# Optimization experiments

Hardware: AMD Instinct MI355X
Metric: run time of the kernel (lower is better)

## Reference

```python
import jax, jax.numpy as jnp
import numpy as np

N_QUBITS = 8
DEPTH = 3
FEATURE_DIM = 512
NUM_CLASSES = 10
BATCH = 8192
CDTYPE = jnp.complex64


def _ry_batched(theta):
    # theta: (B,) -> (B,2,2) real RY matrices cast to complex
    c = jnp.cos(theta / 2)
    s = jnp.sin(theta / 2)
    row0 = jnp.stack([c, -s], axis=-1)
    row1 = jnp.stack([s, c], axis=-1)
    return jnp.stack([row0, row1], axis=-2).astype(CDTYPE)


def _ry(theta):
    c = jnp.cos(theta / 2).astype(CDTYPE)
    s = jnp.sin(theta / 2).astype(CDTYPE)
    return jnp.stack([jnp.stack([c, -s]), jnp.stack([s, c])])


def _rx(theta):
    c = jnp.cos(theta / 2).astype(CDTYPE)
    js = (-1j) * jnp.sin(theta / 2).astype(CDTYPE)
    return jnp.stack([jnp.stack([c, js]), jnp.stack([js, c])])


def _apply_1q(state, U, q, n):
    # state: (B, 2,...,2) little-endian: axis (n - q) holds qubit q's bit
    ax = n - q
    sm = jnp.moveaxis(state, ax, -1)
    if U.ndim == 3:  # per-batch gate
        new = jnp.einsum('b...k,bjk->b...j', sm, U)
    else:  # shared gate
        new = jnp.einsum('...k,jk->...j', sm, U)
    return jnp.moveaxis(new, -1, ax)


def _cnot(state, c, t, n):
    ax_c = n - c
    ax_t = n - t
    s0, s1 = jnp.split(state, 2, axis=ax_c)
    s1 = jnp.flip(s1, axis=ax_t)  # X on target where control=1
    return jnp.concatenate([s0, s1], axis=ax_c)


def _quantum_expect(angles, qnn_w, n=N_QUBITS, depth=DEPTH):
    # angles: (B, n) encoding angles; qnn_w: (depth*n*3,) circuit weights
    B = angles.shape[0]
    state = jnp.zeros((B,) + (2,) * n, CDTYPE)
    state = state.at[(slice(None),) + (0,) * n].set(1.0)
    # RY encoding layer (batched angles)
    for q in range(n):
        state = _apply_1q(state, _ry_batched(angles[:, q]), q, n)
    wr = qnn_w.reshape(depth, n, 3)
    for l in range(depth):
        for q in range(n):
            state = _apply_1q(state, _rx(wr[l, q, 0]), q, n)
            state = _apply_1q(state, _ry(wr[l, q, 1]), q, n)
            state = _apply_1q(state, _rx(wr[l, q, 2]), q, n)
        for q in range(n - 1):
            state = _cnot(state, q, q + 1, n)
        state = _cnot(state, n - 1, 0, n)
    # PauliZ expectation per qubit: sum probs weighted by (+1, -1) on that qubit's axis
    p = state.real ** 2 + state.imag ** 2  # (B, 2,...,2) real
    z = jnp.array([1.0, -1.0], p.dtype)
    outs = []
    for q in range(n):
        ax = n - q
        sign = z.reshape((1,) * ax + (2,) + (1,) * q)
        outs.append(jnp.sum(p * sign, axis=tuple(range(1, n + 1))))
    return jnp.stack(outs, axis=-1)  # (B, n)


def setup_inputs() -> dict:
    key = jax.random.key(0)
    k1, k2, k3, k4, k5 = jax.random.split(key, 5)
    x = jax.random.normal(k1, (BATCH, FEATURE_DIM), jnp.float32)
    bound_p = 1.0 / np.sqrt(FEATURE_DIM)
    proj_w = jax.random.uniform(k2, (N_QUBITS, FEATURE_DIM), jnp.float32, -bound_p, bound_p)
    qnn_w = 0.01 * jax.random.normal(k3, (DEPTH * N_QUBITS * 3,), jnp.float32)
    bound_o = 1.0 / np.sqrt(N_QUBITS)
    out_w = jax.random.uniform(k4, (NUM_CLASSES, N_QUBITS), jnp.float32, -bound_o, bound_o)
    out_b = jax.random.uniform(k5, (NUM_CLASSES,), jnp.float32, -bound_o, bound_o)
    return {'x': x, 'proj_w': proj_w, 'qnn_w': qnn_w, 'out_w': out_w, 'out_b': out_b}


def reference(x, proj_w, qnn_w, out_w, out_b):
    angles = jnp.tanh(x @ proj_w.T) * (jnp.pi / 2)  # (B, n_qubits)
    q_out = _quantum_expect(angles, qnn_w)          # (B, n_qubits)
    return q_out @ out_w.T + out_b                  # (B, num_classes)
```

## Files before the change

### kernel.cpp

```cpp
#include <hip/hip_runtime.h>
#include <math.h>

#define NQ 8
#define NDEPTH 3
#define FEAT 512
#define NCLS 10
#define NBATCH 8192

__global__ void gate_precompute(const float* __restrict__ qnn_w,
                                float* __restrict__ gates) {
    int i = threadIdx.x;
    if (i < NDEPTH * NQ) {
        float t0 = 0.5f * qnn_w[i * 3 + 0];
        float t1 = 0.5f * qnn_w[i * 3 + 1];
        float t2 = 0.5f * qnn_w[i * 3 + 2];
        float c0 = cosf(t0), s0 = sinf(t0);
        float c1 = cosf(t1), s1 = sinf(t1);
        float c2 = cosf(t2), s2 = sinf(t2);
        float m00r =  c1 * c0, m00i =  s1 * s0;
        float m01r = -s1 * c0, m01i = -c1 * s0;
        float m10r =  s1 * c0, m10i = -c1 * s0;
        float m11r =  c1 * c0, m11i = -s1 * s0;
        float* g = gates + i * 8;
        g[0] =  c2 * m00r + s2 * m10i;  g[1] =  c2 * m00i - s2 * m10r;
        g[2] =  c2 * m01r + s2 * m11i;  g[3] =  c2 * m01i - s2 * m11r;
        g[4] =  s2 * m00i + c2 * m10r;  g[5] = -s2 * m00r + c2 * m10i;
        g[6] =  s2 * m01i + c2 * m11r;  g[7] = -s2 * m01r + c2 * m11i;
    }
}

template <int CTRL, int ROW_MASK>
__device__ __forceinline__ float dpp_term(float v) {
    return __int_as_float(__builtin_amdgcn_update_dpp(
        0, __float_as_int(v), CTRL, ROW_MASK, 0xf, true));
}

__device__ __forceinline__ float wave_sum_bcast(float v) {
    v += dpp_term<0x111, 0xf>(v);
    v += dpp_term<0x112, 0xf>(v);
    v += dpp_term<0x114, 0xf>(v);
    v += dpp_term<0x118, 0xf>(v);
    v += dpp_term<0x142, 0xa>(v);
    v += dpp_term<0x143, 0xc>(v);
    return __int_as_float(__builtin_amdgcn_readlane(__float_as_int(v), 63));
}

__device__ __forceinline__ float bcastlane(float v, int srclane) {
    return __int_as_float(__builtin_amdgcn_readlane(__float_as_int(v), srclane));
}

template <int CTRL>
__device__ __forceinline__ float dpp_xor(float v) {
    return __int_as_float(__builtin_amdgcn_update_dpp(
        0, __float_as_int(v), CTRL, 0xf, 0xf, true));
}

__device__ __forceinline__ float fast_tanh(float v) {
    float e = __expf(2.f * v);
    return 1.f - 2.f / (e + 1.f);
}


__device__ __forceinline__ void cgate_pair(const float* __restrict__ u,
        float& r0, float& i0, float& r1, float& i1) {
    float nr0 = u[0]*r0 - u[1]*i0 + u[2]*r1 - u[3]*i1;
    float ni0 = u[0]*i0 + u[1]*r0 + u[2]*i1 + u[3]*r1;
    float nr1 = u[4]*r0 - u[5]*i0 + u[6]*r1 - u[7]*i1;
    float ni1 = u[4]*i0 + u[5]*r0 + u[6]*i1 + u[7]*r1;
    r0 = nr0; i0 = ni0; r1 = nr1; i1 = ni1;
}

__device__ __forceinline__ void cgate_shfl(const float* __restrict__ u, int bit,
        int mask, float (&re)[4], float (&im)[4]) {
    float dr  = bit ? u[6] : u[0], di = bit ? u[7] : u[1];
    float orr = bit ? u[4] : u[2], oi = bit ? u[5] : u[3];
#pragma unroll
    for (int j = 0; j < 4; j++) {
        float pr = __shfl_xor(re[j], mask);
        float pi = __shfl_xor(im[j], mask);
        float nr = dr*re[j] - di*im[j] + orr*pr - oi*pi;
        float ni = dr*im[j] + di*re[j] + orr*pi + oi*pr;
        re[j] = nr; im[j] = ni;
    }
}

template <int CTRL>
__device__ __forceinline__ void cgate_dpp(const float* __restrict__ u, int bit,
        float (&re)[4], float (&im)[4]) {
    float dr  = bit ? u[6] : u[0], di = bit ? u[7] : u[1];
    float orr = bit ? u[4] : u[2], oi = bit ? u[5] : u[3];
#pragma unroll
    for (int j = 0; j < 4; j++) {
        float pr = dpp_xor<CTRL>(re[j]);
        float pi = dpp_xor<CTRL>(im[j]);
        float nr = dr*re[j] - di*im[j] + orr*pr - oi*pi;
        float ni = dr*im[j] + di*re[j] + orr*pi + oi*pr;
        re[j] = nr; im[j] = ni;
    }
}

__global__ __launch_bounds__(256) void qsim_kernel(
        const float* __restrict__ x, const float* __restrict__ proj_w,
        const float* __restrict__ gates, const float* __restrict__ out_w,
        const float* __restrict__ out_b, float* __restrict__ out) {
    int tid  = threadIdx.x;
    int lane = tid & 63;
    int b    = blockIdx.x * 4 + (tid >> 6);

    const float4* xr4 = (const float4*)(x + (size_t)b * FEAT);
    float4 xa = xr4[lane], xb = xr4[lane + 64];
    float dq[8];
#pragma unroll
    for (int q = 0; q < 8; q++) {
        const float4* pw4 = (const float4*)(proj_w + q * FEAT);
        float4 wa = pw4[lane], wb = pw4[lane + 64];
        float acc = xa.x*wa.x + xa.y*wa.y + xa.z*wa.z + xa.w*wa.w
                  + xb.x*wb.x + xb.y*wb.y + xb.z*wb.z + xb.w*wb.w;
        dq[q] = wave_sum_bcast(acc);
    }
    int qsel = lane >> 3;
    float a0 = (qsel & 4) ? dq[4] : dq[0];
    float a1 = (qsel & 4) ? dq[5] : dq[1];
    float a2 = (qsel & 4) ? dq[6] : dq[2];
    float a3 = (qsel & 4) ? dq[7] : dq[3];
    float b0 = (qsel & 2) ? a2 : a0;
    float b1 = (qsel & 2) ? a3 : a1;
    float dsel = (qsel & 1) ? b1 : b0;
    float th = fast_tanh(dsel) * 0.78539816339744830962f;
    float se = __sinf(th), ce = __cosf(th);
    float cq[8], sq[8];
#pragma unroll
    for (int q = 0; q < 8; q++) {
        cq[q] = bcastlane(ce, q * 8);
        sq[q] = bcastlane(se, q * 8);
    }

    float F = 1.f;
#pragma unroll
    for (int q = 2; q < 8; q++) {
        int bit = (lane >> (q - 2)) & 1;
        F *= bit ? sq[q] : cq[q];
    }
    float re[4], im[4];
    re[0] = F * cq[0] * cq[1];
    re[1] = F * sq[0] * cq[1];
    re[2] = F * cq[0] * sq[1];
    re[3] = F * sq[0] * sq[1];
    im[0] = im[1] = im[2] = im[3] = 0.f;

#pragma unroll
    for (int l = 0; l < NDEPTH; l++) {
        const float* g = gates + l * NQ * 8;
        cgate_pair(g, re[0], im[0], re[1], im[1]);
        cgate_pair(g, re[2], im[2], re[3], im[3]);
        cgate_pair(g + 8,  re[0], im[0], re[2], im[2]);
        cgate_pair(g + 8,  re[1], im[1], re[3], im[3]);
        cgate_dpp<0xB1>(g + 16, lane & 1,        re, im);
        cgate_dpp<0x4E>(g + 24, (lane >> 1) & 1, re, im);
        cgate_shfl(g + 32, (lane >> 2) & 1, 4,  re, im);
        cgate_shfl(g + 40, (lane >> 3) & 1, 8,  re, im);
        cgate_shfl(g + 48, (lane >> 4) & 1, 16, re, im);
        cgate_shfl(g + 56, (lane >> 5) & 1, 32, re, im);

        { float t = re[1]; re[1] = re[3]; re[3] = t;
          t = im[1]; im[1] = im[3]; im[3] = t; }
        int base  = lane ^ ((lane << 1) & 63);
        int base2 = base ^ 1;
        re[0] = __shfl(re[0], base);  im[0] = __shfl(im[0], base);
        re[1] = __shfl(re[1], base);  im[1] = __shfl(im[1], base);
        re[2] = __shfl(re[2], base2); im[2] = __shfl(im[2], base2);
        re[3] = __shfl(re[3], base2); im[3] = __shfl(im[3], base2);
        int bit5 = (lane >> 5) & 1;
        {
            float t0 = bit5 ? re[1] : re[0], t1 = bit5 ? re[0] : re[1];
            float t2 = bit5 ? re[3] : re[2], t3 = bit5 ? re[2] : re[3];
            re[0] = t0; re[1] = t1; re[2] = t2; re[3] = t3;
            t0 = bit5 ? im[1] : im[0]; t1 = bit5 ? im[0] : im[1];
            t2 = bit5 ? im[3] : im[2]; t3 = bit5 ? im[2] : im[3];
            im[0] = t0; im[1] = t1; im[2] = t2; im[3] = t3;
        }
    }

    float p0 = re[0]*re[0] + im[0]*im[0];
    float p1 = re[1]*re[1] + im[1]*im[1];
    float p2 = re[2]*re[2] + im[2]*im[2];
    float p3 = re[3]*re[3] + im[3]*im[3];
    float pt = p0 + p1 + p2 + p3;
    float eq[8];
    eq[0] = wave_sum_bcast(p0 - p1 + p2 - p3);
    eq[1] = wave_sum_bcast(p0 + p1 - p2 - p3);
#pragma unroll
    for (int q = 2; q < 8; q++) {
        int bit = (lane >> (q - 2)) & 1;
        eq[q] = wave_sum_bcast(bit ? -pt : pt);
    }

    if (lane < NCLS) {
        const float* wrow = out_w + lane * NQ;
        float acc = out_b[lane];
#pragma unroll
        for (int q = 0; q < 8; q++) acc = fmaf(eq[q], wrow[q], acc);
        out[(size_t)b * NCLS + lane] = acc;
    }
}

extern "C" void kernel_launch(void* const* d_in, const int* in_sizes, int n_in,
                              void* d_out, int out_size, void* d_ws, size_t ws_size,
                              hipStream_t stream) {
    const float* x      = (const float*)d_in[0];
    const float* proj_w = (const float*)d_in[1];
    const float* qnn_w  = (const float*)d_in[2];
    const float* out_w  = (const float*)d_in[3];
    const float* out_b  = (const float*)d_in[4];
    float* out   = (float*)d_out;
    float* gates = (float*)d_ws;

    gate_precompute<<<1, 64, 0, stream>>>(qnn_w, gates);
    qsim_kernel<<<NBATCH / 4, 256, 0, stream>>>(x, proj_w, gates, out_w, out_b, out);
}
```

Baseline: 85.56 us.

## Recast circuit as 256x256 unitary matrix applied via fp16 MFMA GEMM

Splits the fused simulation into four kernels. The first writes product-state encodings to a workspace in fp16. The second builds the full 256x256 circuit unitary by simulating each basis state. The third multiplies the encodings by the unitary's real and imaginary parts on MFMA, then folds the probabilities straight into class logits through a precomputed sign table. This moves the per-sample gate shuffles onto matrix cores, but adds extra launches, a workspace round trip, and fp16 rounding of both the state and the unitary.

```diff
diff --git a/kernel.cpp b/kernel.cpp
--- a/kernel.cpp
+++ b/kernel.cpp
@@ -7,8 +7,14 @@
 #define NCLS 10
 #define NBATCH 8192
 
-__global__ void gate_precompute(const float* __restrict__ qnn_w,
-                                float* __restrict__ gates) {
+typedef _Float16 v8h __attribute__((ext_vector_type(8)));
+typedef _Float16 v4h __attribute__((ext_vector_type(4)));
+typedef float v4f __attribute__((ext_vector_type(4)));
+
+
+__global__ void precompute(const float* __restrict__ qnn_w,
+                           const float* __restrict__ out_w,
+                           float* __restrict__ gates, float* __restrict__ T) {
     int i = threadIdx.x;
     if (i < NDEPTH * NQ) {
         float t0 = 0.5f * qnn_w[i * 3 + 0];
@@ -27,6 +33,16 @@
         g[4] =  s2 * m00i + c2 * m10r;  g[5] = -s2 * m00r + c2 * m10i;
         g[6] =  s2 * m01i + c2 * m11r;  g[7] = -s2 * m01r + c2 * m11i;
     }
+    if (i < 256) {
+#pragma unroll
+        for (int c = 0; c < NCLS; c++) {
+            float s = 0.f;
+#pragma unroll
+            for (int q = 0; q < NQ; q++)
+                s += (((i >> q) & 1) ? -1.f : 1.f) * out_w[c * NQ + q];
+            T[i * NCLS + c] = s;
+        }
+    }
 }
 
 template <int CTRL, int ROW_MASK>
@@ -60,7 +76,6 @@
     return 1.f - 2.f / (e + 1.f);
 }
 
-
 __device__ __forceinline__ void cgate_pair(const float* __restrict__ u,
         float& r0, float& i0, float& r1, float& i1) {
     float nr0 = u[0]*r0 - u[1]*i0 + u[2]*r1 - u[3]*i1;
@@ -99,55 +114,8 @@
     }
 }
 
-__global__ __launch_bounds__(256) void qsim_kernel(
-        const float* __restrict__ x, const float* __restrict__ proj_w,
-        const float* __restrict__ gates, const float* __restrict__ out_w,
-        const float* __restrict__ out_b, float* __restrict__ out) {
-    int tid  = threadIdx.x;
-    int lane = tid & 63;
-    int b    = blockIdx.x * 4 + (tid >> 6);
-
-    const float4* xr4 = (const float4*)(x + (size_t)b * FEAT);
-    float4 xa = xr4[lane], xb = xr4[lane + 64];
-    float dq[8];
-#pragma unroll
-    for (int q = 0; q < 8; q++) {
-        const float4* pw4 = (const float4*)(proj_w + q * FEAT);
-        float4 wa = pw4[lane], wb = pw4[lane + 64];
-        float acc = xa.x*wa.x + xa.y*wa.y + xa.z*wa.z + xa.w*wa.w
-                  + xb.x*wb.x + xb.y*wb.y + xb.z*wb.z + xb.w*wb.w;
-        dq[q] = wave_sum_bcast(acc);
-    }
-    int qsel = lane >> 3;
-    float a0 = (qsel & 4) ? dq[4] : dq[0];
-    float a1 = (qsel & 4) ? dq[5] : dq[1];
-    float a2 = (qsel & 4) ? dq[6] : dq[2];
-    float a3 = (qsel & 4) ? dq[7] : dq[3];
-    float b0 = (qsel & 2) ? a2 : a0;
-    float b1 = (qsel & 2) ? a3 : a1;
-    float dsel = (qsel & 1) ? b1 : b0;
-    float th = fast_tanh(dsel) * 0.78539816339744830962f;
-    float se = __sinf(th), ce = __cosf(th);
-    float cq[8], sq[8];
-#pragma unroll
-    for (int q = 0; q < 8; q++) {
-        cq[q] = bcastlane(ce, q * 8);
-        sq[q] = bcastlane(se, q * 8);
-    }
-
-    float F = 1.f;
-#pragma unroll
-    for (int q = 2; q < 8; q++) {
-        int bit = (lane >> (q - 2)) & 1;
-        F *= bit ? sq[q] : cq[q];
-    }
-    float re[4], im[4];
-    re[0] = F * cq[0] * cq[1];
-    re[1] = F * sq[0] * cq[1];
-    re[2] = F * cq[0] * sq[1];
-    re[3] = F * sq[0] * sq[1];
-    im[0] = im[1] = im[2] = im[3] = 0.f;
-
+__device__ __forceinline__ void apply_circuit(const float* __restrict__ gates,
+        int lane, float (&re)[4], float (&im)[4]) {
 #pragma unroll
     for (int l = 0; l < NDEPTH; l++) {
         const float* g = gates + l * NQ * 8;
@@ -161,7 +129,6 @@
         cgate_shfl(g + 40, (lane >> 3) & 1, 8,  re, im);
         cgate_shfl(g + 48, (lane >> 4) & 1, 16, re, im);
         cgate_shfl(g + 56, (lane >> 5) & 1, 32, re, im);
-
         { float t = re[1]; re[1] = re[3]; re[3] = t;
           t = im[1]; im[1] = im[3]; im[3] = t; }
         int base  = lane ^ ((lane << 1) & 63);
@@ -180,27 +147,143 @@
             im[0] = t0; im[1] = t1; im[2] = t2; im[3] = t3;
         }
     }
-
-    float p0 = re[0]*re[0] + im[0]*im[0];
-    float p1 = re[1]*re[1] + im[1]*im[1];
-    float p2 = re[2]*re[2] + im[2]*im[2];
-    float p3 = re[3]*re[3] + im[3]*im[3];
-    float pt = p0 + p1 + p2 + p3;
-    float eq[8];
-    eq[0] = wave_sum_bcast(p0 - p1 + p2 - p3);
-    eq[1] = wave_sum_bcast(p0 + p1 - p2 - p3);
+}
+
+__global__ __launch_bounds__(256) void enc_kernel(
+        const float* __restrict__ x, const float* __restrict__ proj_w,
+        _Float16* __restrict__ enc) {
+    int tid  = threadIdx.x;
+    int lane = tid & 63;
+    int b    = blockIdx.x * 4 + (tid >> 6);
+
+    const float4* xr4 = (const float4*)(x + (size_t)b * FEAT);
+    float4 xa = xr4[lane], xb = xr4[lane + 64];
+    float dq[8];
+#pragma unroll
+    for (int q = 0; q < 8; q++) {
+        const float4* pw4 = (const float4*)(proj_w + q * FEAT);
+        float4 wa = pw4[lane], wb = pw4[lane + 64];
+        float acc = xa.x*wa.x + xa.y*wa.y + xa.z*wa.z + xa.w*wa.w
+                  + xb.x*wb.x + xb.y*wb.y + xb.z*wb.z + xb.w*wb.w;
+        dq[q] = wave_sum_bcast(acc);
+    }
+    int qsel = lane >> 3;
+    float a0 = (qsel & 4) ? dq[4] : dq[0];
+    float a1 = (qsel & 4) ? dq[5] : dq[1];
+    float a2 = (qsel & 4) ? dq[6] : dq[2];
+    float a3 = (qsel & 4) ? dq[7] : dq[3];
+    float b0 = (qsel & 2) ? a2 : a0;
+    float b1 = (qsel & 2) ? a3 : a1;
+    float dsel = (qsel & 1) ? b1 : b0;
+    float th = fast_tanh(dsel) * 0.78539816339744830962f;
+    float se = __sinf(th), ce = __cosf(th);
+    float cq[8], sq[8];
+#pragma unroll
+    for (int q = 0; q < 8; q++) {
+        cq[q] = bcastlane(ce, q * 8);
+        sq[q] = bcastlane(se, q * 8);
+    }
+    float F = 1.f;
 #pragma unroll
     for (int q = 2; q < 8; q++) {
         int bit = (lane >> (q - 2)) & 1;
-        eq[q] = wave_sum_bcast(bit ? -pt : pt);
-    }
-
-    if (lane < NCLS) {
-        const float* wrow = out_w + lane * NQ;
-        float acc = out_b[lane];
-#pragma unroll
-        for (int q = 0; q < 8; q++) acc = fmaf(eq[q], wrow[q], acc);
-        out[(size_t)b * NCLS + lane] = acc;
+        F *= bit ? sq[q] : cq[q];
+    }
+    v4h ev;
+    ev[0] = (_Float16)(F * cq[0] * cq[1]);
+    ev[1] = (_Float16)(F * sq[0] * cq[1]);
+    ev[2] = (_Float16)(F * cq[0] * sq[1]);
+    ev[3] = (_Float16)(F * sq[0] * sq[1]);
+    *(v4h*)(enc + (size_t)b * 256 + lane * 4) = ev;
+}
+
+__global__ __launch_bounds__(256) void build_w(
+        const float* __restrict__ gates,
+        _Float16* __restrict__ Bre, _Float16* __restrict__ Bim) {
+    int tid  = threadIdx.x;
+    int lane = tid & 63;
+    int p    = blockIdx.x * 4 + (tid >> 6);
+
+    float re[4], im[4];
+#pragma unroll
+    for (int j = 0; j < 4; j++) {
+        re[j] = (lane * 4 + j == p) ? 1.f : 0.f;
+        im[j] = 0.f;
+    }
+    apply_circuit(gates, lane, re, im);
+
+    int t  = lane >> 2;
+    int kk = p >> 5;
+    int qp = (p >> 3) & 3;
+    int j  = p & 7;
+#pragma unroll
+    for (int r = 0; r < 4; r++) {
+        int n15  = (lane & 3) * 4 + r;
+        int flat = ((t * 8 + kk) * 64 + qp * 16 + n15) * 8 + j;
+        Bre[flat] = (_Float16)re[r];
+        Bim[flat] = (_Float16)im[r];
+    }
+}
+
+__global__ __launch_bounds__(64) void gemm_head(
+        const _Float16* __restrict__ enc,
+        const _Float16* __restrict__ Bre, const _Float16* __restrict__ Bim,
+        const float* __restrict__ T, const float* __restrict__ out_b,
+        float* __restrict__ out) {
+    int lane = threadIdx.x;
+    int rowbase = blockIdx.x * 16;
+    int m = lane & 15, quad = lane >> 4;
+
+    v8h a[8];
+#pragma unroll
+    for (int kk = 0; kk < 8; kk++)
+        a[kk] = *(const v8h*)(enc + (size_t)(rowbase + m) * 256 + kk * 32 + quad * 8);
+
+    float oacc[4][NCLS] = {};
+#pragma unroll
+    for (int t = 0; t < 16; t++) {
+        int col = t * 16 + m;
+        float tc[NCLS];
+#pragma unroll
+        for (int c = 0; c < NCLS; c++) tc[c] = T[col * NCLS + c];
+
+        v4f ar = {0.f, 0.f, 0.f, 0.f}, ai = {0.f, 0.f, 0.f, 0.f};
+#pragma unroll
+        for (int kk = 0; kk < 8; kk++) {
+            size_t fb = ((size_t)(t * 8 + kk)) * 512 + (size_t)lane * 8;
+            v8h br = *(const v8h*)(Bre + fb);
+            v8h bi = *(const v8h*)(Bim + fb);
+            ar = __builtin_amdgcn_mfma_f32_16x16x32_f16(a[kk], br, ar, 0, 0, 0);
+            ai = __builtin_amdgcn_mfma_f32_16x16x32_f16(a[kk], bi, ai, 0, 0, 0);
+        }
+#pragma unroll
+        for (int r = 0; r < 4; r++) {
+            float pv = ar[r] * ar[r] + ai[r] * ai[r];
+#pragma unroll
+            for (int c = 0; c < NCLS; c++)
+                oacc[r][c] = fmaf(pv, tc[c], oacc[r][c]);
+        }
+    }
+#pragma unroll
+    for (int r = 0; r < 4; r++) {
+#pragma unroll
+        for (int c = 0; c < NCLS; c++) {
+            float v = oacc[r][c];
+            v += dpp_term<0x111, 0xf>(v);
+            v += dpp_term<0x112, 0xf>(v);
+            v += dpp_term<0x114, 0xf>(v);
+            v += dpp_term<0x118, 0xf>(v);
+            oacc[r][c] = v;
+        }
+    }
+    if (m == 15) {
+#pragma unroll
+        for (int r = 0; r < 4; r++) {
+            int row = rowbase + quad * 4 + r;
+#pragma unroll
+            for (int c = 0; c < NCLS; c++)
+                out[row * NCLS + c] = oacc[r][c] + out_b[c];
+        }
     }
 }
 
@@ -212,9 +295,17 @@
     const float* qnn_w  = (const float*)d_in[2];
     const float* out_w  = (const float*)d_in[3];
     const float* out_b  = (const float*)d_in[4];
-    float* out   = (float*)d_out;
-    float* gates = (float*)d_ws;
-
-    gate_precompute<<<1, 64, 0, stream>>>(qnn_w, gates);
-    qsim_kernel<<<NBATCH / 4, 256, 0, stream>>>(x, proj_w, gates, out_w, out_b, out);
-}
+    float* out = (float*)d_out;
+
+    char* ws = (char*)d_ws;
+    float*     gates = (float*)(ws + 0);
+    float*     T     = (float*)(ws + 4096);
+    _Float16*  Bre   = (_Float16*)(ws + 16384);
+    _Float16*  Bim   = (_Float16*)(ws + 16384 + 131072);
+    _Float16*  enc   = (_Float16*)(ws + 278528);
+
+    precompute<<<1, 256, 0, stream>>>(qnn_w, out_w, gates, T);
+    enc_kernel<<<NBATCH / 4, 256, 0, stream>>>(x, proj_w, enc);
+    build_w<<<64, 256, 0, stream>>>(gates, Bre, Bim);
+    gemm_head<<<NBATCH / 16, 64, 0, stream>>>(enc, Bre, Bim, T, out_b, out);
+}
```

After: 101.3 us. 1.18x slower.
